# Performance work log

Measured on AMD Instinct MI355X. Metric: run time of the kernel, lower is better.

## Reference

```python
import jax, jax.numpy as jnp
import numpy as np

B, N, D_POINTS, D_MODEL = 2, 2048, 32, 512


def _gather(feat, idx):
    # feat: [B, N, C], idx: [B, N, K] -> [B, N, K, C]
    return jax.vmap(lambda f, i: f[i])(feat, idx)


def setup_inputs() -> dict:
    key = jax.random.key(0)
    ks = jax.random.split(key, 20)
    def lin(k, fan_in, fan_out):
        bound = 1.0 / np.sqrt(fan_in)
        return jax.random.uniform(k, (fan_in, fan_out), jnp.float32, -bound, bound)
    def bias(k, fan_in, fan_out):
        bound = 1.0 / np.sqrt(fan_in)
        return jax.random.uniform(k, (fan_out,), jnp.float32, -bound, bound)
    return {
        "xyz": jax.random.normal(ks[0], (B, N, 3), jnp.float32),
        "points": jax.random.normal(ks[1], (B, N, D_POINTS), jnp.float32),
        "fc1_w": lin(ks[2], D_POINTS, D_MODEL), "fc1_b": bias(ks[3], D_POINTS, D_MODEL),
        "fc2_w": lin(ks[4], D_MODEL, D_POINTS), "fc2_b": bias(ks[5], D_MODEL, D_POINTS),
        "delta_w1": lin(ks[6], 3, D_MODEL), "delta_b1": bias(ks[7], 3, D_MODEL),
        "delta_w2": lin(ks[8], D_MODEL, D_MODEL), "delta_b2": bias(ks[9], D_MODEL, D_MODEL),
        "gamma_w1": lin(ks[10], D_MODEL, D_MODEL), "gamma_b1": bias(ks[11], D_MODEL, D_MODEL),
        "gamma_w2": lin(ks[12], D_MODEL, D_MODEL), "gamma_b2": bias(ks[13], D_MODEL, D_MODEL),
        "wq": lin(ks[14], D_MODEL, D_MODEL),
        "wk": lin(ks[15], D_MODEL, D_MODEL),
        "wv": lin(ks[16], D_MODEL, D_MODEL),
        "knn_k": 16,
    }


def reference(xyz, points, fc1_w, fc1_b, fc2_w, fc2_b,
              delta_w1, delta_b1, delta_w2, delta_b2,
              gamma_w1, gamma_b1, gamma_w2, gamma_b2,
              wq, wk, wv, knn_k):
    # square_distance: [B, N, N]
    sq = jnp.sum(xyz * xyz, axis=-1)
    dists = sq[:, :, None] + sq[:, None, :] - 2.0 * jnp.einsum('bnc,bmc->bnm', xyz, xyz)
    # knn: k smallest distances (argsort[:, :, :k] equivalent)
    _, knn_idx = jax.lax.top_k(-dists, knn_k)           # [B, N, K]
    knn_xyz = _gather(xyz, knn_idx)                      # [B, N, K, 3]

    pre = points
    x = points @ fc1_w + fc1_b                           # [B, N, d_model]
    q = x @ wq                                           # [B, N, d_model]
    k = _gather(x @ wk, knn_idx)                         # [B, N, K, d_model]
    v = _gather(x @ wv, knn_idx)                         # [B, N, K, d_model]

    # positional encoding MLP on delta xyz
    delta = xyz[:, :, None, :] - knn_xyz                 # [B, N, K, 3]
    pos_enc = jax.nn.relu(delta @ delta_w1 + delta_b1) @ delta_w2 + delta_b2

    # gamma MLP on (q - k + pos_enc)
    a = q[:, :, None, :] - k + pos_enc
    a = jax.nn.relu(a @ gamma_w1 + gamma_b1) @ gamma_w2 + gamma_b2

    scale = jnp.asarray(np.sqrt(D_MODEL), a.dtype)
    attn = jax.nn.softmax(a / scale, axis=-2)            # softmax over neighbors, per channel

    res = jnp.sum(attn * (v + pos_enc), axis=2)          # einsum 'bmnf,bmnf->bmf'
    res = res @ fc2_w + fc2_b + pre                      # [B, N, d_points]
    return res, attn
```

## Files before the change

### kernel.cpp

```cpp
#include <hip/hip_runtime.h>
#include <hip/hip_bf16.h>
#include <math.h>

typedef __bf16 bf16_t;
typedef float f32x4 __attribute__((ext_vector_type(4)));
typedef bf16_t bf16x8 __attribute__((ext_vector_type(8)));

#define BM 128
#define BN 128
#define BKT 64

#define GLD_LDS16(gp, lp) __builtin_amdgcn_global_load_lds( \
    (const __attribute__((address_space(1))) void*)(gp), \
    (__attribute__((address_space(3))) void*)(lp), 16, 0, 0)

struct TC6 { const float* src[6]; bf16_t* dst[6]; };
__global__ __launch_bounds__(256) void tcast6_kernel(TC6 tc) {
  int job = blockIdx.x >> 10;
  int idx = (blockIdx.x & 1023) * 256 + threadIdx.x;
  int n = idx >> 9, k = idx & 511;
  tc.dst[job][idx] = (bf16_t)tc.src[job][k * 512 + n];
}

__global__ __launch_bounds__(256) void knn_kernel(const float* __restrict__ xyz, int* __restrict__ knn) {
  __shared__ float sx[2048], sy[2048], sz[2048], sq[2048];
  int tid = threadIdx.x;
  int lane = tid & 63, wave = tid >> 6;
  int gq = blockIdx.x * 4 + wave;
  int b  = gq >> 11;
  int base = b << 11;
  for (int p = tid; p < 2048; p += 256) {
    float x = xyz[(base + p) * 3 + 0];
    float y = xyz[(base + p) * 3 + 1];
    float z = xyz[(base + p) * 3 + 2];
    sx[p] = x; sy[p] = y; sz[p] = z;
    sq[p] = __fadd_rn(__fadd_rn(__fmul_rn(x, x), __fmul_rn(y, y)), __fmul_rn(z, z));
  }
  __syncthreads();
  int iq = gq & 2047;
  float qx = sx[iq], qy = sy[iq], qz = sz[iq], sqi = sq[iq];

  unsigned long long key[32];
  #pragma unroll
  for (int j = 0; j < 32; ++j) {
    int p = lane + j * 64;
    float d = __fmul_rn(sx[p], qx);
    d = fmaf(sy[p], qy, d);
    d = fmaf(sz[p], qz, d);
    float dist = __fsub_rn(__fadd_rn(sqi, sq[p]), __fmul_rn(2.0f, d));
    unsigned int bits = __float_as_uint(dist);
    unsigned int sk = bits ^ (unsigned int)(((int)bits >> 31) | 0x80000000);
    key[j] = ((unsigned long long)sk << 32) | (unsigned int)p;
  }

  int r = 0;
  #pragma unroll 1
  for (int s = 0; s < 16; ++s) {
    unsigned long long m = key[0];
    #pragma unroll
    for (int j = 1; j < 32; ++j) m = (key[j] < m) ? key[j] : m;
    #pragma unroll
    for (int off = 32; off > 0; off >>= 1) {
      unsigned long long o = (unsigned long long)__shfl_xor((long long)m, off);
      if (o < m) m = o;
    }
    if (lane == s) r = base + (int)(m & 0xFFFFFFFFu);
    #pragma unroll
    for (int j = 0; j < 32; ++j) key[j] = (key[j] == m) ? ~0ULL : key[j];
  }
  if (lane < 16) knn[gq * 16 + lane] = r;
}

__global__ __launch_bounds__(256) void xfeat_kernel(const float* __restrict__ points, const float* __restrict__ fc1_w,
                                                    const float* __restrict__ fc1_b, bf16_t* __restrict__ xb) {
  __shared__ float p[32];
  int m = blockIdx.x, tid = threadIdx.x;
  if (tid < 32) p[tid] = points[m * 32 + tid];
  __syncthreads();
  for (int c = tid; c < 512; c += 256) {
    float a = fc1_b[c];
    #pragma unroll
    for (int kk = 0; kk < 32; ++kk) a = fmaf(p[kk], fc1_w[kk * 512 + c], a);
    xb[m * 512 + c] = (bf16_t)a;
  }
}

__global__ __launch_bounds__(256) void h1_kernel(const float* __restrict__ xyz, const int* __restrict__ knn,
                                                 const float* __restrict__ dw1, const float* __restrict__ db1,
                                                 bf16_t* __restrict__ h1) {
  __shared__ float w0[512], w1r[512], w2[512], bb[512];
  int g = blockIdx.x, tid = threadIdx.x;
  for (int c = tid; c < 512; c += 256) {
    w0[c] = dw1[c]; w1r[c] = dw1[512 + c]; w2[c] = dw1[1024 + c]; bb[c] = db1[c];
  }
  float xi0 = xyz[g * 3 + 0], xi1 = xyz[g * 3 + 1], xi2 = xyz[g * 3 + 2];
  __syncthreads();
  for (int slot = 0; slot < 16; ++slot) {
    int j = knn[g * 16 + slot];
    float d0 = xi0 - xyz[j * 3 + 0];
    float d1 = xi1 - xyz[j * 3 + 1];
    float d2 = xi2 - xyz[j * 3 + 2];
    int m = g * 16 + slot;
    for (int c = tid; c < 512; c += 256) {
      float h = fmaf(d2, w2[c], fmaf(d1, w1r[c], d0 * w0[c])) + bb[c];
      h1[m * 512 + c] = (bf16_t)fmaxf(h, 0.0f);
    }
  }
}

__global__ __launch_bounds__(256) void final_kernel(const float* __restrict__ res_mid, const float* __restrict__ fc2_w,
                                                    const float* __restrict__ fc2_b, const float* __restrict__ points,
                                                    float* __restrict__ out) {
  int oid = blockIdx.x * 256 + threadIdx.x;
  int m = oid >> 5, c = oid & 31;
  float a = fc2_b[c];
  const float* rm = res_mid + m * 512;
  for (int kk = 0; kk < 512; ++kk) a = fmaf(rm[kk], fc2_w[kk * 32 + c], a);
  out[oid] = a + points[oid];
}

template <int SRC, int EPI>
__global__ __launch_bounds__(256) void gemm_kernel(
    const bf16_t* __restrict__ A, const bf16_t* __restrict__ Bt,
    float* __restrict__ Cf, bf16_t* __restrict__ Cb,
    const float* __restrict__ bias, int ldc,
    const float* __restrict__ qkv, float* pe_attn,
    const int* __restrict__ knn, float* __restrict__ res_mid)
{
  __shared__ bf16_t Alds[BM * BKT];
  __shared__ bf16_t Blds[BN * BKT];
  int tid  = threadIdx.x;
  int lane = tid & 63, wave = tid >> 6;
  int wr = wave >> 1, wc = wave & 1;
  int lr = lane & 15, lg = lane >> 4;

  int gx = gridDim.x;
  int nwg = gx * gridDim.y;
  int orig = blockIdx.y * gx + blockIdx.x;
  int cpx = nwg >> 3;
  int swz = (orig & 7) * cpx + (orig >> 3);
  int bx = swz % gx;
  int by = swz / gx;
  int n0 = bx * BN, m0 = by * BM;

  f32x4 acc[4][4];
  #pragma unroll
  for (int i = 0; i < 4; ++i)
    #pragma unroll
    for (int j = 0; j < 4; ++j) acc[i][j] = (f32x4){0.f, 0.f, 0.f, 0.f};

  int srow = tid >> 3;
  int sc8  = (tid & 7) * 8;

  for (int k0 = 0; k0 < 512; k0 += BKT) {
    if (SRC == 0) {
      #pragma unroll
      for (int it = 0; it < 4; ++it) {
        int r = it * 32 + srow;
        GLD_LDS16(A + (size_t)(m0 + r) * 512 + k0 + sc8, Alds + (it * 4 + wave) * 512);
      }
    } else {
      #pragma unroll
      for (int it = 0; it < 4; ++it) {
        int r = it * 32 + srow;
        int m = m0 + r;
        int g = m >> 4;
        int j = knn[m];
        const float* qp = qkv + (size_t)g * 1536 + k0 + sc8;
        const float* kp = qkv + (size_t)j * 1536 + 512 + k0 + sc8;
        const float* pp = pe_attn + (size_t)m * 512 + k0 + sc8;
        f32x4 q0 = *(const f32x4*)qp,  q1 = *(const f32x4*)(qp + 4);
        f32x4 k0v = *(const f32x4*)kp, k1v = *(const f32x4*)(kp + 4);
        f32x4 p0 = *(const f32x4*)pp,  p1 = *(const f32x4*)(pp + 4);
        bf16x8 o;
        #pragma unroll
        for (int u = 0; u < 4; ++u) o[u] = (bf16_t)(q0[u] - k0v[u] + p0[u]);
        #pragma unroll
        for (int u = 0; u < 4; ++u) o[4 + u] = (bf16_t)(q1[u] - k1v[u] + p1[u]);
        *(bf16x8*)(&Alds[r * BKT + sc8]) = o;
      }
    }
    #pragma unroll
    for (int it = 0; it < 4; ++it) {
      int r = it * 32 + srow;
      GLD_LDS16(Bt + (size_t)(n0 + r) * 512 + k0 + sc8, Blds + (it * 4 + wave) * 512);
    }
    __syncthreads();
    #pragma unroll
    for (int kk = 0; kk < BKT; kk += 32) {
      int ko = kk + 8 * lg;
      bf16x8 af[4], bfr[4];
      #pragma unroll
      for (int mi = 0; mi < 4; ++mi) af[mi] = *(const bf16x8*)(&Alds[(wr * 64 + mi * 16 + lr) * BKT + ko]);
      #pragma unroll
      for (int nj = 0; nj < 4; ++nj) bfr[nj] = *(const bf16x8*)(&Blds[(wc * 64 + nj * 16 + lr) * BKT + ko]);
      #pragma unroll
      for (int mi = 0; mi < 4; ++mi)
        #pragma unroll
        for (int nj = 0; nj < 4; ++nj)
          acc[mi][nj] = __builtin_amdgcn_mfma_f32_16x16x32_bf16(af[mi], bfr[nj], acc[mi][nj], 0, 0, 0);
    }
    __syncthreads();
  }

  if (EPI == 0 || EPI == 1) {
    #pragma unroll
    for (int mi = 0; mi < 4; ++mi)
      #pragma unroll
      for (int nj = 0; nj < 4; ++nj) {
        int col = n0 + wc * 64 + nj * 16 + lr;
        #pragma unroll
        for (int r = 0; r < 4; ++r) {
          int row = m0 + wr * 64 + mi * 16 + lg * 4 + r;
          float v = acc[mi][nj][r];
          if (EPI == 1) v += bias[col];
          Cf[(size_t)row * ldc + col] = v;
        }
      }
  } else if (EPI == 2) {
    #pragma unroll
    for (int mi = 0; mi < 4; ++mi)
      #pragma unroll
      for (int nj = 0; nj < 4; ++nj) {
        int col = n0 + wc * 64 + nj * 16 + lr;
        #pragma unroll
        for (int r = 0; r < 4; ++r) {
          int row = m0 + wr * 64 + mi * 16 + lg * 4 + r;
          Cb[(size_t)row * ldc + col] = (bf16_t)fmaxf(acc[mi][nj][r] + bias[col], 0.0f);
        }
      }
  } else {
    const float scale = 22.62741699796952f;
    #pragma unroll
    for (int mi = 0; mi < 4; ++mi) {
      int g = (m0 + wr * 64 + mi * 16) >> 4;
      #pragma unroll
      for (int nj = 0; nj < 4; ++nj) {
        int col = n0 + wc * 64 + nj * 16 + lr;
        float sv[4];
        float mx = -INFINITY;
        #pragma unroll
        for (int r = 0; r < 4; ++r) {
          sv[r] = (acc[mi][nj][r] + bias[col]) / scale;
          mx = fmaxf(mx, sv[r]);
        }
        mx = fmaxf(mx, __shfl_xor(mx, 16));
        mx = fmaxf(mx, __shfl_xor(mx, 32));
        float e[4], sum = 0.f;
        #pragma unroll
        for (int r = 0; r < 4; ++r) { e[r] = expf(sv[r] - mx); sum += e[r]; }
        sum += __shfl_xor(sum, 16);
        sum += __shfl_xor(sum, 32);
        float part = 0.f;
        #pragma unroll
        for (int r = 0; r < 4; ++r) {
          int row = g * 16 + lg * 4 + r;
          float at = e[r] / sum;
          int j = knn[row];
          float vv  = qkv[(size_t)j * 1536 + 1024 + col];
          float pev = pe_attn[(size_t)row * 512 + col];
          part = fmaf(at, vv + pev, part);
          pe_attn[(size_t)row * 512 + col] = at;
        }
        part += __shfl_xor(part, 16);
        part += __shfl_xor(part, 32);
        if (lg == 0) res_mid[(size_t)g * 512 + col] = part;
      }
    }
  }
}

extern "C" void kernel_launch(void* const* d_in, const int* in_sizes, int n_in,
                              void* d_out, int out_size, void* d_ws, size_t ws_size,
                              hipStream_t stream) {
  const float* xyz    = (const float*)d_in[0];
  const float* points = (const float*)d_in[1];
  const float* fc1_w  = (const float*)d_in[2];
  const float* fc1_b  = (const float*)d_in[3];
  const float* fc2_w  = (const float*)d_in[4];
  const float* fc2_b  = (const float*)d_in[5];
  const float* dw1    = (const float*)d_in[6];
  const float* db1    = (const float*)d_in[7];
  const float* dw2    = (const float*)d_in[8];
  const float* db2    = (const float*)d_in[9];
  const float* gw1    = (const float*)d_in[10];
  const float* gb1    = (const float*)d_in[11];
  const float* gw2    = (const float*)d_in[12];
  const float* gb2    = (const float*)d_in[13];
  const float* wq     = (const float*)d_in[14];
  const float* wk     = (const float*)d_in[15];
  const float* wv     = (const float*)d_in[16];

  float* out = (float*)d_out;
  float* attn_pe = out + 131072;

  char* w = (char*)d_ws;
  bf16_t* wqkvT  = (bf16_t*)w; w += (size_t)1536 * 512 * 2;
  bf16_t* dw2T   = (bf16_t*)w; w += (size_t)512 * 512 * 2;
  bf16_t* gw1T   = (bf16_t*)w; w += (size_t)512 * 512 * 2;
  bf16_t* gw2T   = (bf16_t*)w; w += (size_t)512 * 512 * 2;
  int*    knn    = (int*)w;    w += (size_t)65536 * 4;
  bf16_t* xb     = (bf16_t*)w; w += (size_t)4096 * 512 * 2;
  float*  qkv    = (float*)w;  w += (size_t)4096 * 1536 * 4;
  bf16_t* h12    = (bf16_t*)w; w += (size_t)65536 * 512 * 2;
  float*  res_mid= (float*)w;  w += (size_t)4096 * 512 * 4;

  TC6 tc;
  tc.src[0] = wq;  tc.dst[0] = wqkvT;
  tc.src[1] = wk;  tc.dst[1] = wqkvT + 512 * 512;
  tc.src[2] = wv;  tc.dst[2] = wqkvT + 2 * 512 * 512;
  tc.src[3] = dw2; tc.dst[3] = dw2T;
  tc.src[4] = gw1; tc.dst[4] = gw1T;
  tc.src[5] = gw2; tc.dst[5] = gw2T;
  tcast6_kernel<<<6144, 256, 0, stream>>>(tc);

  knn_kernel<<<1024, 256, 0, stream>>>(xyz, knn);
  xfeat_kernel<<<4096, 256, 0, stream>>>(points, fc1_w, fc1_b, xb);

  gemm_kernel<0, 0><<<dim3(12, 32), 256, 0, stream>>>(xb, wqkvT, qkv, nullptr, nullptr, 1536,
                                                      nullptr, nullptr, nullptr, nullptr);
  h1_kernel<<<4096, 256, 0, stream>>>(xyz, knn, dw1, db1, h12);

  gemm_kernel<0, 1><<<dim3(4, 512), 256, 0, stream>>>(h12, dw2T, attn_pe, nullptr, db2, 512,
                                                      nullptr, nullptr, nullptr, nullptr);

  gemm_kernel<1, 2><<<dim3(4, 512), 256, 0, stream>>>(nullptr, gw1T, nullptr, h12, gb1, 512,
                                                      qkv, attn_pe, knn, nullptr);

  gemm_kernel<0, 3><<<dim3(4, 512), 256, 0, stream>>>(h12, gw2T, nullptr, nullptr, gb2, 512,
                                                      qkv, attn_pe, knn, res_mid);

  final_kernel<<<512, 256, 0, stream>>>(res_mid, fc2_w, fc2_b, points, out);
}
```

Measured before the change: 432.9 us.

## Double-buffer GEMM LDS tiles and XOR-swizzle LDS layout

Doubles the LDS buffers in the bf16 MFMA GEMM so the next K-tile is prefetched (async global->LDS for B and A, register prefetch for the fused q-k+pe A path) while the current tile is computed. This halves the barriers per iteration. It also applies an XOR swizzle to the LDS column index to reduce bank conflicts on fragment reads. LDS use doubles to 64KB per block, which may cut occupancy, and the SRC=1 path holds 24 extra f32x4 registers across the MFMA loop.

```diff
diff --git a/kernel.cpp b/kernel.cpp
--- a/kernel.cpp
+++ b/kernel.cpp
@@ -127,8 +127,8 @@
     const float* __restrict__ qkv, float* pe_attn,
     const int* __restrict__ knn, float* __restrict__ res_mid)
 {
-  __shared__ bf16_t Alds[BM * BKT];
-  __shared__ bf16_t Blds[BN * BKT];
+  __shared__ bf16_t Alds[2 * BM * BKT];
+  __shared__ bf16_t Blds[2 * BN * BKT];
   int tid  = threadIdx.x;
   int lane = tid & 63, wave = tid >> 6;
   int wr = wave >> 1, wc = wave & 1;
@@ -149,56 +149,107 @@
     #pragma unroll
     for (int j = 0; j < 4; ++j) acc[i][j] = (f32x4){0.f, 0.f, 0.f, 0.f};
 
-  int srow = tid >> 3;
-  int sc8  = (tid & 7) * 8;
-
-  for (int k0 = 0; k0 < 512; k0 += BKT) {
-    if (SRC == 0) {
-      #pragma unroll
-      for (int it = 0; it < 4; ++it) {
-        int r = it * 32 + srow;
-        GLD_LDS16(A + (size_t)(m0 + r) * 512 + k0 + sc8, Alds + (it * 4 + wave) * 512);
-      }
-    } else {
-      #pragma unroll
-      for (int it = 0; it < 4; ++it) {
-        int r = it * 32 + srow;
-        int m = m0 + r;
-        int g = m >> 4;
-        int j = knn[m];
-        const float* qp = qkv + (size_t)g * 1536 + k0 + sc8;
-        const float* kp = qkv + (size_t)j * 1536 + 512 + k0 + sc8;
-        const float* pp = pe_attn + (size_t)m * 512 + k0 + sc8;
-        f32x4 q0 = *(const f32x4*)qp,  q1 = *(const f32x4*)(qp + 4);
-        f32x4 k0v = *(const f32x4*)kp, k1v = *(const f32x4*)(kp + 4);
-        f32x4 p0 = *(const f32x4*)pp,  p1 = *(const f32x4*)(pp + 4);
-        bf16x8 o;
-        #pragma unroll
-        for (int u = 0; u < 4; ++u) o[u] = (bf16_t)(q0[u] - k0v[u] + p0[u]);
-        #pragma unroll
-        for (int u = 0; u < 4; ++u) o[4 + u] = (bf16_t)(q1[u] - k1v[u] + p1[u]);
-        *(bf16x8*)(&Alds[r * BKT + sc8]) = o;
-      }
-    }
+  int rS  = tid >> 3;
+  int sc8 = (tid & 7) << 3;
+  int scS = (((tid & 7) ^ ((tid >> 3) & 7)) << 3);
+
+  if (SRC == 0) {
+    #pragma unroll
+    for (int it = 0; it < 4; ++it)
+      GLD_LDS16(A + (size_t)(m0 + it * 32 + rS) * 512 + scS, Alds + (it * 4 + wave) * 512);
+  } else {
     #pragma unroll
     for (int it = 0; it < 4; ++it) {
-      int r = it * 32 + srow;
-      GLD_LDS16(Bt + (size_t)(n0 + r) * 512 + k0 + sc8, Blds + (it * 4 + wave) * 512);
-    }
-    __syncthreads();
+      int r = it * 32 + rS;
+      int m = m0 + r;
+      int g = m >> 4;
+      int j = knn[m];
+      const float* qp = qkv + (size_t)g * 1536 + sc8;
+      const float* kp = qkv + (size_t)j * 1536 + 512 + sc8;
+      const float* pp = pe_attn + (size_t)m * 512 + sc8;
+      f32x4 q0 = *(const f32x4*)qp,  q1 = *(const f32x4*)(qp + 4);
+      f32x4 k0v = *(const f32x4*)kp, k1v = *(const f32x4*)(kp + 4);
+      f32x4 p0 = *(const f32x4*)pp,  p1 = *(const f32x4*)(pp + 4);
+      bf16x8 o;
+      #pragma unroll
+      for (int u = 0; u < 4; ++u) o[u] = (bf16_t)(q0[u] - k0v[u] + p0[u]);
+      #pragma unroll
+      for (int u = 0; u < 4; ++u) o[4 + u] = (bf16_t)(q1[u] - k1v[u] + p1[u]);
+      *(bf16x8*)(&Alds[r * BKT + scS]) = o;
+    }
+  }
+  #pragma unroll
+  for (int it = 0; it < 4; ++it)
+    GLD_LDS16(Bt + (size_t)(n0 + it * 32 + rS) * 512 + scS, Blds + (it * 4 + wave) * 512);
+  __syncthreads();
+
+  #pragma unroll 1
+  for (int t = 0; t < 8; ++t) {
+    int cur = t & 1;
+    int k0n = (t + 1) * BKT;
+
+    f32x4 pq0[4], pq1[4], pk0[4], pk1[4], pp0[4], pp1[4];
+    if (t < 7) {
+      if (SRC == 0) {
+        bf16_t* Ab = Alds + (cur ^ 1) * (BM * BKT);
+        #pragma unroll
+        for (int it = 0; it < 4; ++it)
+          GLD_LDS16(A + (size_t)(m0 + it * 32 + rS) * 512 + k0n + scS, Ab + (it * 4 + wave) * 512);
+      } else {
+        #pragma unroll
+        for (int it = 0; it < 4; ++it) {
+          int m = m0 + it * 32 + rS;
+          int g = m >> 4;
+          int j = knn[m];
+          const float* qp = qkv + (size_t)g * 1536 + k0n + sc8;
+          const float* kp = qkv + (size_t)j * 1536 + 512 + k0n + sc8;
+          const float* pp = pe_attn + (size_t)m * 512 + k0n + sc8;
+          pq0[it] = *(const f32x4*)qp;  pq1[it] = *(const f32x4*)(qp + 4);
+          pk0[it] = *(const f32x4*)kp;  pk1[it] = *(const f32x4*)(kp + 4);
+          pp0[it] = *(const f32x4*)pp;  pp1[it] = *(const f32x4*)(pp + 4);
+        }
+      }
+      bf16_t* Bb = Blds + (cur ^ 1) * (BN * BKT);
+      #pragma unroll
+      for (int it = 0; it < 4; ++it)
+        GLD_LDS16(Bt + (size_t)(n0 + it * 32 + rS) * 512 + k0n + scS, Bb + (it * 4 + wave) * 512);
+    }
+
+    const bf16_t* Ab = Alds + cur * (BM * BKT);
+    const bf16_t* Bb = Blds + cur * (BN * BKT);
     #pragma unroll
     for (int kk = 0; kk < BKT; kk += 32) {
-      int ko = kk + 8 * lg;
+      int ks = (kk >> 3) + lg;
       bf16x8 af[4], bfr[4];
       #pragma unroll
-      for (int mi = 0; mi < 4; ++mi) af[mi] = *(const bf16x8*)(&Alds[(wr * 64 + mi * 16 + lr) * BKT + ko]);
-      #pragma unroll
-      for (int nj = 0; nj < 4; ++nj) bfr[nj] = *(const bf16x8*)(&Blds[(wc * 64 + nj * 16 + lr) * BKT + ko]);
+      for (int mi = 0; mi < 4; ++mi) {
+        int rr = wr * 64 + mi * 16 + lr;
+        af[mi] = *(const bf16x8*)(&Ab[rr * BKT + ((ks ^ (rr & 7)) << 3)]);
+      }
+      #pragma unroll
+      for (int nj = 0; nj < 4; ++nj) {
+        int rr = wc * 64 + nj * 16 + lr;
+        bfr[nj] = *(const bf16x8*)(&Bb[rr * BKT + ((ks ^ (rr & 7)) << 3)]);
+      }
       #pragma unroll
       for (int mi = 0; mi < 4; ++mi)
         #pragma unroll
         for (int nj = 0; nj < 4; ++nj)
           acc[mi][nj] = __builtin_amdgcn_mfma_f32_16x16x32_bf16(af[mi], bfr[nj], acc[mi][nj], 0, 0, 0);
+    }
+
+    if (SRC == 1 && t < 7) {
+      bf16_t* Ab2 = Alds + (cur ^ 1) * (BM * BKT);
+      #pragma unroll
+      for (int it = 0; it < 4; ++it) {
+        int r = it * 32 + rS;
+        bf16x8 o;
+        #pragma unroll
+        for (int u = 0; u < 4; ++u) o[u] = (bf16_t)(pq0[it][u] - pk0[it][u] + pp0[it][u]);
+        #pragma unroll
+        for (int u = 0; u < 4; ++u) o[4 + u] = (bf16_t)(pq1[it][u] - pk1[it][u] + pp1[it][u]);
+        *(bf16x8*)(&Ab2[r * BKT + scS]) = o;
+      }
     }
     __syncthreads();
   }
```

After: 457.5 us. 5.7% more time.

## Fold gamma_w1 through linear layers and fuse h1 generation into pos-enc GEMM

Applied to the files above, without the earlier changes.

Uses linearity to precompute Wp = delta_w2·gamma_w1, q·gamma_w1 and k·gamma_w1 at point level, plus a folded bias. The gamma first layer then becomes a second accumulator inside the pos-enc GEMM rather than a separate 65536-row GEMM fed by gathered q-k+pe. The h1 relu features are computed on the fly in the GEMM A-tile loader instead of being written to and read from HBM. LDS tiles get XOR swizzling and intermediates are stored in bf16. The cost is extra bf16 rounding of the folded weights and the qk projections, plus higher register and LDS use from the dual accumulator.

```diff
diff --git a/kernel.cpp b/kernel.cpp
--- a/kernel.cpp
+++ b/kernel.cpp
@@ -14,12 +14,24 @@
     (const __attribute__((address_space(1))) void*)(gp), \
     (__attribute__((address_space(3))) void*)(lp), 16, 0, 0)
 
-struct TC6 { const float* src[6]; bf16_t* dst[6]; };
-__global__ __launch_bounds__(256) void tcast6_kernel(TC6 tc) {
+struct TC7 { const float* src[7]; bf16_t* dst[7]; };
+__global__ __launch_bounds__(256) void tcast7_kernel(TC7 tc) {
   int job = blockIdx.x >> 10;
   int idx = (blockIdx.x & 1023) * 256 + threadIdx.x;
-  int n = idx >> 9, k = idx & 511;
-  tc.dst[job][idx] = (bf16_t)tc.src[job][k * 512 + n];
+  if (job < 6) {
+    int n = idx >> 9, k = idx & 511;
+    tc.dst[job][idx] = (bf16_t)tc.src[job][k * 512 + n];
+  } else {
+    tc.dst[job][idx] = (bf16_t)tc.src[job][idx];
+  }
+}
+
+__global__ __launch_bounds__(256) void cc_kernel(const float* __restrict__ db2, const float* __restrict__ gw1,
+                                                 const float* __restrict__ gb1, float* __restrict__ cc) {
+  int n = blockIdx.x * 256 + threadIdx.x;
+  float s = gb1[n];
+  for (int d = 0; d < 512; ++d) s = fmaf(db2[d], gw1[d * 512 + n], s);
+  cc[n] = s;
 }
 
 __global__ __launch_bounds__(256) void knn_kernel(const float* __restrict__ xyz, int* __restrict__ knn) {
@@ -85,29 +97,6 @@
   }
 }
 
-__global__ __launch_bounds__(256) void h1_kernel(const float* __restrict__ xyz, const int* __restrict__ knn,
-                                                 const float* __restrict__ dw1, const float* __restrict__ db1,
-                                                 bf16_t* __restrict__ h1) {
-  __shared__ float w0[512], w1r[512], w2[512], bb[512];
-  int g = blockIdx.x, tid = threadIdx.x;
-  for (int c = tid; c < 512; c += 256) {
-    w0[c] = dw1[c]; w1r[c] = dw1[512 + c]; w2[c] = dw1[1024 + c]; bb[c] = db1[c];
-  }
-  float xi0 = xyz[g * 3 + 0], xi1 = xyz[g * 3 + 1], xi2 = xyz[g * 3 + 2];
-  __syncthreads();
-  for (int slot = 0; slot < 16; ++slot) {
-    int j = knn[g * 16 + slot];
-    float d0 = xi0 - xyz[j * 3 + 0];
-    float d1 = xi1 - xyz[j * 3 + 1];
-    float d2 = xi2 - xyz[j * 3 + 2];
-    int m = g * 16 + slot;
-    for (int c = tid; c < 512; c += 256) {
-      float h = fmaf(d2, w2[c], fmaf(d1, w1r[c], d0 * w0[c])) + bb[c];
-      h1[m * 512 + c] = (bf16_t)fmaxf(h, 0.0f);
-    }
-  }
-}
-
 __global__ __launch_bounds__(256) void final_kernel(const float* __restrict__ res_mid, const float* __restrict__ fc2_w,
                                                     const float* __restrict__ fc2_b, const float* __restrict__ points,
                                                     float* __restrict__ out) {
@@ -119,16 +108,19 @@
   out[oid] = a + points[oid];
 }
 
+struct GP {
+  const bf16_t* A; const bf16_t* Bt; const bf16_t* Bt2;
+  bf16_t* Cb; const float* bias; int ldc;
+  const float* xyz; const int* knn; const float* dw1; const float* db1;
+  const float* cc; const bf16_t* qkg; float* pe; bf16_t* h2;
+  const bf16_t* vb; float* pe_attn; float* res_mid;
+};
+
 template <int SRC, int EPI>
-__global__ __launch_bounds__(256) void gemm_kernel(
-    const bf16_t* __restrict__ A, const bf16_t* __restrict__ Bt,
-    float* __restrict__ Cf, bf16_t* __restrict__ Cb,
-    const float* __restrict__ bias, int ldc,
-    const float* __restrict__ qkv, float* pe_attn,
-    const int* __restrict__ knn, float* __restrict__ res_mid)
-{
+__global__ __launch_bounds__(256) void gemm_kernel(GP gp) {
   __shared__ bf16_t Alds[BM * BKT];
   __shared__ bf16_t Blds[BN * BKT];
+  __shared__ bf16_t B2lds[(EPI == 5) ? (BN * BKT) : 8];
   int tid  = threadIdx.x;
   int lane = tid & 63, wave = tid >> 6;
   int wr = wave >> 1, wc = wave & 1;
@@ -144,66 +136,99 @@
   int n0 = bx * BN, m0 = by * BM;
 
   f32x4 acc[4][4];
+  f32x4 acc2[4][4];
   #pragma unroll
   for (int i = 0; i < 4; ++i)
     #pragma unroll
-    for (int j = 0; j < 4; ++j) acc[i][j] = (f32x4){0.f, 0.f, 0.f, 0.f};
-
-  int srow = tid >> 3;
-  int sc8  = (tid & 7) * 8;
-
+    for (int j = 0; j < 4; ++j) {
+      acc[i][j] = (f32x4){0.f, 0.f, 0.f, 0.f};
+      if (EPI == 5) acc2[i][j] = (f32x4){0.f, 0.f, 0.f, 0.f};
+    }
+
+  int rS  = tid >> 3;
+  int sc8 = (tid & 7) << 3;
+  int scS = (((tid & 7) ^ ((tid >> 3) & 7)) << 3);
+
+  float dx[4], dy[4], dz[4];
+  if (SRC == 2) {
+    #pragma unroll
+    for (int it = 0; it < 4; ++it) {
+      int m = m0 + it * 32 + rS;
+      int g = m >> 4;
+      int j = gp.knn[m];
+      dx[it] = gp.xyz[g * 3 + 0] - gp.xyz[j * 3 + 0];
+      dy[it] = gp.xyz[g * 3 + 1] - gp.xyz[j * 3 + 1];
+      dz[it] = gp.xyz[g * 3 + 2] - gp.xyz[j * 3 + 2];
+    }
+  }
+
+  #pragma unroll 1
   for (int k0 = 0; k0 < 512; k0 += BKT) {
     if (SRC == 0) {
       #pragma unroll
+      for (int it = 0; it < 4; ++it)
+        GLD_LDS16(gp.A + (size_t)(m0 + it * 32 + rS) * 512 + k0 + scS, Alds + (it * 4 + wave) * 512);
+    } else {
+      const float* w0p = gp.dw1 + k0 + sc8;
+      f32x4 w0a = *(const f32x4*)w0p,          w0b = *(const f32x4*)(w0p + 4);
+      f32x4 w1a = *(const f32x4*)(w0p + 512),  w1b = *(const f32x4*)(w0p + 516);
+      f32x4 w2a = *(const f32x4*)(w0p + 1024), w2b = *(const f32x4*)(w0p + 1028);
+      const float* bbp = gp.db1 + k0 + sc8;
+      f32x4 bba = *(const f32x4*)bbp,          bbb = *(const f32x4*)(bbp + 4);
+      #pragma unroll
       for (int it = 0; it < 4; ++it) {
-        int r = it * 32 + srow;
-        GLD_LDS16(A + (size_t)(m0 + r) * 512 + k0 + sc8, Alds + (it * 4 + wave) * 512);
-      }
-    } else {
-      #pragma unroll
-      for (int it = 0; it < 4; ++it) {
-        int r = it * 32 + srow;
-        int m = m0 + r;
-        int g = m >> 4;
-        int j = knn[m];
-        const float* qp = qkv + (size_t)g * 1536 + k0 + sc8;
-        const float* kp = qkv + (size_t)j * 1536 + 512 + k0 + sc8;
-        const float* pp = pe_attn + (size_t)m * 512 + k0 + sc8;
-        f32x4 q0 = *(const f32x4*)qp,  q1 = *(const f32x4*)(qp + 4);
-        f32x4 k0v = *(const f32x4*)kp, k1v = *(const f32x4*)(kp + 4);
-        f32x4 p0 = *(const f32x4*)pp,  p1 = *(const f32x4*)(pp + 4);
         bf16x8 o;
         #pragma unroll
-        for (int u = 0; u < 4; ++u) o[u] = (bf16_t)(q0[u] - k0v[u] + p0[u]);
-        #pragma unroll
-        for (int u = 0; u < 4; ++u) o[4 + u] = (bf16_t)(q1[u] - k1v[u] + p1[u]);
-        *(bf16x8*)(&Alds[r * BKT + sc8]) = o;
-      }
-    }
-    #pragma unroll
-    for (int it = 0; it < 4; ++it) {
-      int r = it * 32 + srow;
-      GLD_LDS16(Bt + (size_t)(n0 + r) * 512 + k0 + sc8, Blds + (it * 4 + wave) * 512);
+        for (int u = 0; u < 4; ++u) {
+          float h = fmaf(dz[it], w2a[u], fmaf(dy[it], w1a[u], dx[it] * w0a[u])) + bba[u];
+          o[u] = (bf16_t)fmaxf(h, 0.0f);
+        }
+        #pragma unroll
+        for (int u = 0; u < 4; ++u) {
+          float h = fmaf(dz[it], w2b[u], fmaf(dy[it], w1b[u], dx[it] * w0b[u])) + bbb[u];
+          o[4 + u] = (bf16_t)fmaxf(h, 0.0f);
+        }
+        *(bf16x8*)(&Alds[(it * 32 + rS) * BKT + scS]) = o;
+      }
+    }
+    #pragma unroll
+    for (int it = 0; it < 4; ++it)
+      GLD_LDS16(gp.Bt + (size_t)(n0 + it * 32 + rS) * 512 + k0 + scS, Blds + (it * 4 + wave) * 512);
+    if (EPI == 5) {
+      #pragma unroll
+      for (int it = 0; it < 4; ++it)
+        GLD_LDS16(gp.Bt2 + (size_t)(n0 + it * 32 + rS) * 512 + k0 + scS, B2lds + (it * 4 + wave) * 512);
     }
     __syncthreads();
+
     #pragma unroll
     for (int kk = 0; kk < BKT; kk += 32) {
-      int ko = kk + 8 * lg;
-      bf16x8 af[4], bfr[4];
-      #pragma unroll
-      for (int mi = 0; mi < 4; ++mi) af[mi] = *(const bf16x8*)(&Alds[(wr * 64 + mi * 16 + lr) * BKT + ko]);
-      #pragma unroll
-      for (int nj = 0; nj < 4; ++nj) bfr[nj] = *(const bf16x8*)(&Blds[(wc * 64 + nj * 16 + lr) * BKT + ko]);
+      int ks = (kk >> 3) + lg;
+      bf16x8 af[4], bfr[4], b2r[4];
+      #pragma unroll
+      for (int mi = 0; mi < 4; ++mi) {
+        int rr = wr * 64 + mi * 16 + lr;
+        af[mi] = *(const bf16x8*)(&Alds[rr * BKT + ((ks ^ (rr & 7)) << 3)]);
+      }
+      #pragma unroll
+      for (int nj = 0; nj < 4; ++nj) {
+        int rr = wc * 64 + nj * 16 + lr;
+        bfr[nj] = *(const bf16x8*)(&Blds[rr * BKT + ((ks ^ (rr & 7)) << 3)]);
+        if (EPI == 5) b2r[nj] = *(const bf16x8*)(&B2lds[rr * BKT + ((ks ^ (rr & 7)) << 3)]);
+      }
       #pragma unroll
       for (int mi = 0; mi < 4; ++mi)
         #pragma unroll
-        for (int nj = 0; nj < 4; ++nj)
+        for (int nj = 0; nj < 4; ++nj) {
           acc[mi][nj] = __builtin_amdgcn_mfma_f32_16x16x32_bf16(af[mi], bfr[nj], acc[mi][nj], 0, 0, 0);
+          if (EPI == 5)
+            acc2[mi][nj] = __builtin_amdgcn_mfma_f32_16x16x32_bf16(af[mi], b2r[nj], acc2[mi][nj], 0, 0, 0);
+        }
     }
     __syncthreads();
   }
 
-  if (EPI == 0 || EPI == 1) {
+  if (EPI == 4) {
     #pragma unroll
     for (int mi = 0; mi < 4; ++mi)
       #pragma unroll
@@ -212,23 +237,55 @@
         #pragma unroll
         for (int r = 0; r < 4; ++r) {
           int row = m0 + wr * 64 + mi * 16 + lg * 4 + r;
-          float v = acc[mi][nj][r];
-          if (EPI == 1) v += bias[col];
-          Cf[(size_t)row * ldc + col] = v;
-        }
-      }
-  } else if (EPI == 2) {
+          gp.Cb[(size_t)col * 512 + row] = (bf16_t)acc[mi][nj][r];
+        }
+      }
+  } else if (EPI == 6) {
     #pragma unroll
     for (int mi = 0; mi < 4; ++mi)
       #pragma unroll
       for (int nj = 0; nj < 4; ++nj) {
         int col = n0 + wc * 64 + nj * 16 + lr;
+        int part = col >> 9, c = col & 511;
         #pragma unroll
         for (int r = 0; r < 4; ++r) {
           int row = m0 + wr * 64 + mi * 16 + lg * 4 + r;
-          Cb[(size_t)row * ldc + col] = (bf16_t)fmaxf(acc[mi][nj][r] + bias[col], 0.0f);
-        }
-      }
+          gp.Cb[((size_t)part * 4096 + row) * 512 + c] = (bf16_t)acc[mi][nj][r];
+        }
+      }
+  } else if (EPI == 7) {
+    #pragma unroll
+    for (int mi = 0; mi < 4; ++mi)
+      #pragma unroll
+      for (int nj = 0; nj < 4; ++nj) {
+        int col = n0 + wc * 64 + nj * 16 + lr;
+        #pragma unroll
+        for (int r = 0; r < 4; ++r) {
+          int row = m0 + wr * 64 + mi * 16 + lg * 4 + r;
+          gp.Cb[(size_t)row * gp.ldc + col] = (bf16_t)acc[mi][nj][r];
+        }
+      }
+  } else if (EPI == 5) {
+    #pragma unroll
+    for (int mi = 0; mi < 4; ++mi) {
+      int g = (m0 + wr * 64 + mi * 16) >> 4;
+      #pragma unroll
+      for (int nj = 0; nj < 4; ++nj) {
+        int col = n0 + wc * 64 + nj * 16 + lr;
+        float db2v = gp.bias[col];
+        float ccv  = gp.cc[col];
+        float qgv  = (float)gp.qkg[(size_t)g * 512 + col];
+        #pragma unroll
+        for (int r = 0; r < 4; ++r) {
+          int row = m0 + wr * 64 + mi * 16 + lg * 4 + r;
+          gp.pe[(size_t)row * 512 + col] = acc[mi][nj][r] + db2v;
+          int j = gp.knn[row];
+          float kgv = (float)gp.qkg[(size_t)(4096 + j) * 512 + col];
+          float hv = acc2[mi][nj][r] + ccv + qgv - kgv;
+          gp.h2[(size_t)row * 512 + col] = (bf16_t)fmaxf(hv, 0.0f);
+        }
+      }
+    }
   } else {
     const float scale = 22.62741699796952f;
     #pragma unroll
@@ -241,7 +298,7 @@
         float mx = -INFINITY;
         #pragma unroll
         for (int r = 0; r < 4; ++r) {
-          sv[r] = (acc[mi][nj][r] + bias[col]) / scale;
+          sv[r] = (acc[mi][nj][r] + gp.bias[col]) / scale;
           mx = fmaxf(mx, sv[r]);
         }
         mx = fmaxf(mx, __shfl_xor(mx, 16));
@@ -256,15 +313,15 @@
         for (int r = 0; r < 4; ++r) {
           int row = g * 16 + lg * 4 + r;
           float at = e[r] / sum;
-          int j = knn[row];
-          float vv  = qkv[(size_t)j * 1536 + 1024 + col];
-          float pev = pe_attn[(size_t)row * 512 + col];
+          int j = gp.knn[row];
+          float vv  = (float)gp.vb[(size_t)j * 512 + col];
+          float pev = gp.pe_attn[(size_t)row * 512 + col];
           part = fmaf(at, vv + pev, part);
-          pe_attn[(size_t)row * 512 + col] = at;
+          gp.pe_attn[(size_t)row * 512 + col] = at;
         }
         part += __shfl_xor(part, 16);
         part += __shfl_xor(part, 32);
-        if (lg == 0) res_mid[(size_t)g * 512 + col] = part;
+        if (lg == 0) gp.res_mid[(size_t)g * 512 + col] = part;
       }
     }
   }
@@ -299,36 +356,52 @@
   bf16_t* dw2T   = (bf16_t*)w; w += (size_t)512 * 512 * 2;
   bf16_t* gw1T   = (bf16_t*)w; w += (size_t)512 * 512 * 2;
   bf16_t* gw2T   = (bf16_t*)w; w += (size_t)512 * 512 * 2;
+  bf16_t* dw2b   = (bf16_t*)w; w += (size_t)512 * 512 * 2;
+  bf16_t* WpT    = (bf16_t*)w; w += (size_t)512 * 512 * 2;
+  float*  cc     = (float*)w;  w += (size_t)512 * 4;
   int*    knn    = (int*)w;    w += (size_t)65536 * 4;
   bf16_t* xb     = (bf16_t*)w; w += (size_t)4096 * 512 * 2;
-  float*  qkv    = (float*)w;  w += (size_t)4096 * 1536 * 4;
-  bf16_t* h12    = (bf16_t*)w; w += (size_t)65536 * 512 * 2;
+  bf16_t* qkvb   = (bf16_t*)w; w += (size_t)3 * 4096 * 512 * 2;
+  bf16_t* qkg    = (bf16_t*)w; w += (size_t)2 * 4096 * 512 * 2;
+  bf16_t* h2     = (bf16_t*)w; w += (size_t)65536 * 512 * 2;
   float*  res_mid= (float*)w;  w += (size_t)4096 * 512 * 4;
 
-  TC6 tc;
+  TC7 tc;
   tc.src[0] = wq;  tc.dst[0] = wqkvT;
   tc.src[1] = wk;  tc.dst[1] = wqkvT + 512 * 512;
   tc.src[2] = wv;  tc.dst[2] = wqkvT + 2 * 512 * 512;
   tc.src[3] = dw2; tc.dst[3] = dw2T;
   tc.src[4] = gw1; tc.dst[4] = gw1T;
   tc.src[5] = gw2; tc.dst[5] = gw2T;
-  tcast6_kernel<<<6144, 256, 0, stream>>>(tc);
+  tc.src[6] = dw2; tc.dst[6] = dw2b;
+  tcast7_kernel<<<7168, 256, 0, stream>>>(tc);
 
   knn_kernel<<<1024, 256, 0, stream>>>(xyz, knn);
   xfeat_kernel<<<4096, 256, 0, stream>>>(points, fc1_w, fc1_b, xb);
-
-  gemm_kernel<0, 0><<<dim3(12, 32), 256, 0, stream>>>(xb, wqkvT, qkv, nullptr, nullptr, 1536,
-                                                      nullptr, nullptr, nullptr, nullptr);
-  h1_kernel<<<4096, 256, 0, stream>>>(xyz, knn, dw1, db1, h12);
-
-  gemm_kernel<0, 1><<<dim3(4, 512), 256, 0, stream>>>(h12, dw2T, attn_pe, nullptr, db2, 512,
-                                                      nullptr, nullptr, nullptr, nullptr);
-
-  gemm_kernel<1, 2><<<dim3(4, 512), 256, 0, stream>>>(nullptr, gw1T, nullptr, h12, gb1, 512,
-                                                      qkv, attn_pe, knn, nullptr);
-
-  gemm_kernel<0, 3><<<dim3(4, 512), 256, 0, stream>>>(h12, gw2T, nullptr, nullptr, gb2, 512,
-                                                      qkv, attn_pe, knn, res_mid);
+  cc_kernel<<<2, 256, 0, stream>>>(db2, gw1, gb1, cc);
+
+  GP gp{};
+  gp.A = dw2b; gp.Bt = gw1T; gp.Cb = WpT; gp.ldc = 512;
+  gemm_kernel<0, 4><<<dim3(4, 4), 256, 0, stream>>>(gp);
+
+  GP gq{};
+  gq.A = xb; gq.Bt = wqkvT; gq.Cb = qkvb; gq.ldc = 1536;
+  gemm_kernel<0, 6><<<dim3(12, 32), 256, 0, stream>>>(gq);
+
+  GP gk{};
+  gk.A = qkvb; gk.Bt = gw1T; gk.Cb = qkg; gk.ldc = 512;
+  gemm_kernel<0, 7><<<dim3(4, 64), 256, 0, stream>>>(gk);
+
+  GP gd{};
+  gd.Bt = dw2T; gd.Bt2 = WpT; gd.bias = db2;
+  gd.xyz = xyz; gd.knn = knn; gd.dw1 = dw1; gd.db1 = db1;
+  gd.cc = cc; gd.qkg = qkg; gd.pe = attn_pe; gd.h2 = h2;
+  gemm_kernel<2, 5><<<dim3(4, 512), 256, 0, stream>>>(gd);
+
+  GP gs{};
+  gs.A = h2; gs.Bt = gw2T; gs.bias = gb2;
+  gs.knn = knn; gs.vb = qkvb + (size_t)2 * 4096 * 512; gs.pe_attn = attn_pe; gs.res_mid = res_mid;
+  gemm_kernel<0, 3><<<dim3(4, 512), 256, 0, stream>>>(gs);
 
   final_kernel<<<512, 256, 0, stream>>>(res_mid, fc2_w, fc2_b, points, out);
 }
```

Result: slower. 514.4 us (+18.8%).
